# Kernel optimization log

Measured on AMD Instinct MI355X. Metric: run time of the kernel, lower is better.

## Reference

```python
import jax, jax.numpy as jnp
import numpy as np

N = 100000      # nodes
E = 1600000     # edges (before self-loops)
IN = 256        # in_channels
H = 4           # heads (layer 1)
C = 16          # hidden_channels
OUT = 40        # out_channels
NEG_SLOPE = 0.2  # PyG GATConv default


def setup_inputs() -> dict:
    key = jax.random.key(0)
    ks = jax.random.split(key, 10)
    x = jax.random.normal(ks[0], (N, IN), dtype=jnp.float32)
    edge_index = jax.random.randint(ks[1], (2, E), 0, N, dtype=jnp.int64)
    s = 0.1
    return {
        "x": x,
        "edge_index": edge_index,
        "W1": jax.random.normal(ks[2], (IN, H * C), dtype=jnp.float32) * s,
        "a_src1": jax.random.normal(ks[3], (H, C), dtype=jnp.float32) * s,
        "a_dst1": jax.random.normal(ks[4], (H, C), dtype=jnp.float32) * s,
        "b1": jnp.zeros((H * C,), dtype=jnp.float32),
        "W2": jax.random.normal(ks[5], (H * C, OUT), dtype=jnp.float32) * s,
        "a_src2": jax.random.normal(ks[6], (1, OUT), dtype=jnp.float32) * s,
        "a_dst2": jax.random.normal(ks[7], (1, OUT), dtype=jnp.float32) * s,
        "b2": jnp.zeros((OUT,), dtype=jnp.float32),
    }


def gat_conv(x, src, dst, W, a_s, a_d, b, heads, ch, n):
    # x: [n, d_in] -> projected [n, heads, ch]
    xp = (x @ W).reshape(n, heads, ch)
    # per-node attention contributions [n, heads]
    e_s = jnp.einsum('nhc,hc->nh', xp, a_s)
    e_d = jnp.einsum('nhc,hc->nh', xp, a_d)
    # per-edge logits (gather) [E, heads]
    e = jax.nn.leaky_relu(e_s[src] + e_d[dst], negative_slope=NEG_SLOPE)
    # segment softmax over edges sharing a destination node
    m = jax.ops.segment_max(e, dst, num_segments=n)
    m = jnp.where(jnp.isfinite(m), m, 0.0)
    ex = jnp.exp(e - m[dst])
    z = jax.ops.segment_sum(ex, dst, num_segments=n)
    alpha = ex / (z[dst] + 1e-16)               # [E, heads]
    # weighted scatter-add aggregation [n, heads, ch]
    out = jax.ops.segment_sum(xp[src] * alpha[:, :, None], dst, num_segments=n)
    return out.reshape(n, heads * ch) + b       # concat heads + bias


def reference(x, edge_index, W1, a_src1, a_dst1, b1, W2, a_src2, a_dst2, b2):
    n = x.shape[0]
    loop = jnp.arange(n, dtype=edge_index.dtype)
    src = jnp.concatenate([edge_index[0], loop])  # PyG add_self_loops=True
    dst = jnp.concatenate([edge_index[1], loop])
    h = gat_conv(x, src, dst, W1, a_src1, a_dst1, b1, H, C, n)
    h = jax.nn.relu(h)
    out = gat_conv(h, src, dst, W2, a_src2, a_dst2, b2, 1, OUT, n)
    return out
```

## Files before the change

kernel.cpp:

```cpp
#include <hip/hip_runtime.h>
#include <hip/hip_bf16.h>

#define IN_DIM 256
#define HC     64
#define OUT_DIM 40
#define NEG    0.2f

#define NB_SH   8
#define NB_MASK 255
#define SRC_BITS 17
#define SRC_MASK 0x1FFFF
#define CHUNK   8192
#define LEN_CAP 6144

typedef __bf16 bf16x8 __attribute__((ext_vector_type(8)));
typedef float  f32x4  __attribute__((ext_vector_type(4)));

__device__ inline float lrelu(float v) { return fmaxf(v, NEG * v); }

__global__ __launch_bounds__(256) void hist_kernel(
    const int* __restrict__ ei, int* __restrict__ blkhistT, int* __restrict__ btot,
    int E, int ET, int nbuck, int nblk) {
  __shared__ int hist[512];
  int tid = threadIdx.x;
  hist[tid] = 0; hist[tid + 256] = 0;
  __syncthreads();
  int base = blockIdx.x * CHUNK;
  #pragma unroll
  for (int it = 0; it < CHUNK / 1024; ++it) {
    int e = base + it * 1024 + tid * 4;
    if (e + 3 < E) {
      int4 d4 = *(const int4*)&ei[E + e];
      atomicAdd(&hist[d4.x >> NB_SH], 1);
      atomicAdd(&hist[d4.y >> NB_SH], 1);
      atomicAdd(&hist[d4.z >> NB_SH], 1);
      atomicAdd(&hist[d4.w >> NB_SH], 1);
    } else {
      #pragma unroll
      for (int k = 0; k < 4; ++k) {
        int ee = e + k;
        if (ee < ET) {
          int d = (ee < E) ? ei[E + ee] : (ee - E);
          atomicAdd(&hist[d >> NB_SH], 1);
        }
      }
    }
  }
  __syncthreads();
  for (int i = tid; i < nbuck; i += 256) {
    int c = hist[i];
    blkhistT[(size_t)i * nblk + blockIdx.x] = c;
    if (c) atomicAdd(&btot[i], c);
  }
}

__global__ __launch_bounds__(512) void bscan_kernel(
    const int* __restrict__ btot, int* __restrict__ bstart,
    int* __restrict__ offs, int nbuck, int ET, int n) {
  __shared__ int sm[512];
  int tid = threadIdx.x;
  int total = (tid < nbuck) ? btot[tid] : 0;
  sm[tid] = total; __syncthreads();
  for (int o = 1; o < 512; o <<= 1) {
    int v = (tid >= o) ? sm[tid - o] : 0;
    __syncthreads();
    sm[tid] += v;
    __syncthreads();
  }
  if (tid < nbuck) bstart[tid] = sm[tid] - total;
  if (tid == 0) { bstart[nbuck] = ET; offs[n] = ET; }
}

__global__ __launch_bounds__(256) void curs_kernel(
    const int* __restrict__ blkhistT, const int* __restrict__ bstart,
    int* __restrict__ cur, int nblk, int nbuck) {
  __shared__ int sm[256];
  int b = blockIdx.x, tid = threadIdx.x;
  int run = bstart[b];
  for (int c = 0; c < nblk; c += 256) {
    int idx = c + tid;
    int v = (idx < nblk) ? blkhistT[(size_t)b * nblk + idx] : 0;
    sm[tid] = v; __syncthreads();
    for (int o = 1; o < 256; o <<= 1) {
      int x = (tid >= o) ? sm[tid - o] : 0;
      __syncthreads();
      sm[tid] += x;
      __syncthreads();
    }
    if (idx < nblk) cur[(size_t)idx * nbuck + b] = run + sm[tid] - v;
    run += sm[255];
    __syncthreads();
  }
}

__device__ __forceinline__ void gemm1_body(
    char* smem, int tile,
    const float* __restrict__ x, const __bf16* __restrict__ Wt,
    const float* __restrict__ a_s, const float* __restrict__ a_d,
    __bf16* __restrict__ xp1b, float* __restrict__ es1, float* __restrict__ ed1, int n) {
  uint4* wl = (uint4*)smem;
  int tid = threadIdx.x;
  const uint4* gw = (const uint4*)Wt;
  #pragma unroll
  for (int it = 0; it < 4; ++it) {
    int c16 = it * 512 + tid;
    int row = c16 >> 5;
    int swz = c16 ^ (row & 7);
    wl[swz] = gw[c16];
  }
  __syncthreads();

  int wave = tid >> 6, lane = tid & 63;
  int l15 = lane & 15, kgrp = lane >> 4;
  int rowA = tile * 128 + wave * 16 + l15;
  bool okA = rowA < n;
  const float* xrow = x + (size_t)(okA ? rowA : (n - 1)) * IN_DIM;

  f32x4 va[8][2];
  #pragma unroll
  for (int c = 0; c < 8; ++c) {
    int k0 = c * 32 + kgrp * 8;
    va[c][0] = *(const f32x4*)(xrow + k0);
    va[c][1] = *(const f32x4*)(xrow + k0 + 4);
  }
  __builtin_amdgcn_sched_barrier(0);

  f32x4 acc[4] = {};
  #pragma unroll
  for (int c = 0; c < 8; ++c) {
    bf16x8 ahi, alo;
    #pragma unroll
    for (int i = 0; i < 4; ++i) {
      float f0 = va[c][0][i], f1 = va[c][1][i];
      __bf16 h0 = (__bf16)f0, h1 = (__bf16)f1;
      ahi[i]     = h0;
      ahi[4 + i] = h1;
      alo[i]     = (__bf16)(f0 - (float)h0);
      alo[4 + i] = (__bf16)(f1 - (float)h1);
    }
    #pragma unroll
    for (int t = 0; t < 4; ++t) {
      int row  = t * 16 + l15;
      int unit = row * 32 + c * 4 + kgrp;
      int swz  = unit ^ (row & 7);
      bf16x8 b = *(const bf16x8*)&wl[swz];
      acc[t] = __builtin_amdgcn_mfma_f32_16x16x32_bf16(ahi, b, acc[t], 0, 0, 0);
      acc[t] = __builtin_amdgcn_mfma_f32_16x16x32_bf16(alo, b, acc[t], 0, 0, 0);
    }
  }

  int rowbase = tile * 128 + wave * 16 + kgrp * 4;
  #pragma unroll
  for (int t = 0; t < 4; ++t) {
    float as_v = a_s[t * 16 + l15], ad_v = a_d[t * 16 + l15];
    #pragma unroll
    for (int r = 0; r < 4; ++r) {
      int row = rowbase + r;
      float v = acc[t][r];
      bool ok = row < n;
      if (ok) xp1b[(size_t)row * HC + t * 16 + l15] = (__bf16)v;
      float ps = v * as_v, pd = v * ad_v;
      #pragma unroll
      for (int o = 1; o < 16; o <<= 1) {
        ps += __shfl_xor(ps, o, 16);
        pd += __shfl_xor(pd, o, 16);
      }
      if (ok && l15 == 0) {
        es1[row * 4 + t] = ps;
        ed1[row * 4 + t] = pd;
      }
    }
  }
}

__global__ __launch_bounds__(512) void fused_sg(
    const int* __restrict__ ei, const int* __restrict__ cur,
    unsigned int* __restrict__ pairs, int E, int ET, int nbuck, int nsc,
    const float* __restrict__ x, const __bf16* __restrict__ Wt,
    const float* __restrict__ a_s, const float* __restrict__ a_d,
    __bf16* __restrict__ xp1b, float* __restrict__ es1, float* __restrict__ ed1, int n) {
  __shared__ __align__(16) char smem[71680];
  if ((int)blockIdx.x >= nsc) {
    gemm1_body(smem, (int)blockIdx.x - nsc, x, Wt, a_s, a_d, xp1b, es1, ed1, n);
    return;
  }
  int* hs   = (int*)smem;
  int* addb = (int*)(smem + 2048);
  int* lcnt = (int*)(smem + 4096);
  unsigned int* lout = (unsigned int*)(smem + 6144);
  int* ldst = (int*)(smem + 6144 + CHUNK * 4);
  int tid = threadIdx.x, blk = blockIdx.x, base = blk * CHUNK;
  hs[tid] = 0; lcnt[tid] = 0;
  __syncthreads();
  int se[16], de[16];
  #pragma unroll
  for (int it = 0; it < CHUNK / 2048; ++it) {
    int e = base + it * 2048 + tid * 4;
    if (e + 3 < E) {
      int4 s4 = *(const int4*)&ei[e];
      int4 d4 = *(const int4*)&ei[E + e];
      se[it * 4 + 0] = s4.x; de[it * 4 + 0] = d4.x; atomicAdd(&hs[d4.x >> NB_SH], 1);
      se[it * 4 + 1] = s4.y; de[it * 4 + 1] = d4.y; atomicAdd(&hs[d4.y >> NB_SH], 1);
      se[it * 4 + 2] = s4.z; de[it * 4 + 2] = d4.z; atomicAdd(&hs[d4.z >> NB_SH], 1);
      se[it * 4 + 3] = s4.w; de[it * 4 + 3] = d4.w; atomicAdd(&hs[d4.w >> NB_SH], 1);
    } else {
      #pragma unroll
      for (int k = 0; k < 4; ++k) {
        int ee = e + k;
        int s = 0, d = 0;
        if (ee < ET) {
          if (ee < E) { s = ei[ee]; d = ei[E + ee]; }
          else        { s = ee - E; d = s; }
          atomicAdd(&hs[d >> NB_SH], 1);
        }
        se[it * 4 + k] = s; de[it * 4 + k] = d;
      }
    }
  }
  __syncthreads();
  int t = hs[tid];
  for (int o = 1; o < 512; o <<= 1) {
    int v = (tid >= o) ? hs[tid - o] : 0;
    __syncthreads();
    hs[tid] += v;
    __syncthreads();
  }
  int lofs = hs[tid] - t;
  __syncthreads();
  hs[tid] = lofs;
  addb[tid] = ((tid < nbuck) ? cur[(size_t)blk * nbuck + tid] : 0) - lofs;
  __syncthreads();
  #pragma unroll
  for (int it = 0; it < CHUNK / 2048; ++it) {
    #pragma unroll
    for (int k = 0; k < 4; ++k) {
      int e = base + it * 2048 + tid * 4 + k;
      if (e < ET) {
        int b = de[it * 4 + k] >> NB_SH;
        int pos = hs[b] + atomicAdd(&lcnt[b], 1);
        lout[pos] = (unsigned)se[it * 4 + k] |
                    ((unsigned)(de[it * 4 + k] & NB_MASK) << SRC_BITS);
        ldst[pos] = addb[b] + pos;
      }
    }
  }
  __syncthreads();
  int len = min(CHUNK, ET - base);
  for (int i = tid; i < len; i += 512) pairs[ldst[i]] = lout[i];
}

__global__ __launch_bounds__(512) void fused_pg(
    const unsigned int* __restrict__ pairs, const int* __restrict__ bstart,
    int* __restrict__ offs, int* __restrict__ srcs, int n, int nbuck, int tile0,
    const float* __restrict__ x, const __bf16* __restrict__ Wt,
    const float* __restrict__ a_s, const float* __restrict__ a_d,
    __bf16* __restrict__ xp1b, float* __restrict__ es1, float* __restrict__ ed1) {
  __shared__ __align__(16) char smem[53248];
  if ((int)blockIdx.x >= nbuck) {
    gemm1_body(smem, tile0 + (int)blockIdx.x - nbuck, x, Wt, a_s, a_d, xp1b, es1, ed1, n);
    return;
  }
  unsigned int* lin = (unsigned int*)smem;
  unsigned int* lou = (unsigned int*)(smem + 24576);
  int* lhs  = (int*)(smem + 49152);
  int* lcnt = (int*)(smem + 50176);
  int* sm   = (int*)(smem + 51200);
  int b = blockIdx.x, tid = threadIdx.x;
  int rbeg = bstart[b], rend = bstart[b + 1], len = rend - rbeg;
  int node0 = b << NB_SH;
  int nloc = min(256, n - node0);
  if (tid < 256) { lhs[tid] = 0; lcnt[tid] = 0; }
  __syncthreads();
  if (len <= LEN_CAP) {
    for (int i = tid; i < len; i += 512) {
      unsigned p = pairs[rbeg + i];
      lin[i] = p;
      atomicAdd(&lhs[(p >> SRC_BITS) & NB_MASK], 1);
    }
    __syncthreads();
    int t = (tid < 256) ? lhs[tid] : 0;
    sm[tid] = t; __syncthreads();
    for (int o = 1; o < 512; o <<= 1) {
      int v = (tid >= o) ? sm[tid - o] : 0;
      __syncthreads();
      sm[tid] += v;
      __syncthreads();
    }
    int excl = sm[tid] - t;
    if (tid < nloc) offs[node0 + tid] = rbeg + excl;
    if (tid < 256) lhs[tid] = excl;
    __syncthreads();
    for (int i = tid; i < len; i += 512) {
      unsigned p = lin[i];
      int dl = (p >> SRC_BITS) & NB_MASK;
      int pos = lhs[dl] + atomicAdd(&lcnt[dl], 1);
      lou[pos] = p & SRC_MASK;
    }
    __syncthreads();
    for (int i = tid; i < len; i += 512) srcs[rbeg + i] = (int)lou[i];
  } else {
    for (int i = tid; i < len; i += 512)
      atomicAdd(&lhs[(pairs[rbeg + i] >> SRC_BITS) & NB_MASK], 1);
    __syncthreads();
    int t = (tid < 256) ? lhs[tid] : 0;
    sm[tid] = t; __syncthreads();
    for (int o = 1; o < 512; o <<= 1) {
      int v = (tid >= o) ? sm[tid - o] : 0;
      __syncthreads();
      sm[tid] += v;
      __syncthreads();
    }
    int excl = sm[tid] - t;
    if (tid < nloc) offs[node0 + tid] = rbeg + excl;
    if (tid < 256) lhs[tid] = excl;
    __syncthreads();
    for (int i = tid; i < len; i += 512) {
      unsigned p = pairs[rbeg + i];
      int dl = (p >> SRC_BITS) & NB_MASK;
      int pos = lhs[dl] + atomicAdd(&lcnt[dl], 1);
      srcs[rbeg + pos] = (int)(p & SRC_MASK);
    }
  }
}

__global__ void wprep_kernel(const float* __restrict__ W1, __bf16* __restrict__ Wt,
                             int* __restrict__ btot, int nbuck) {
  int i = blockIdx.x * blockDim.x + threadIdx.x;
  if (i < nbuck) btot[i] = 0;
  if (i >= IN_DIM * HC) return;
  int k = i >> 6, nn = i & 63;
  Wt[nn * IN_DIM + k] = (__bf16)W1[i];
}

__global__ __launch_bounds__(256) void agg1_csr(
    const int* __restrict__ offs, const int* __restrict__ srcs,
    const float* __restrict__ es1, const float* __restrict__ ed1,
    const __bf16* __restrict__ xp1b, const float* __restrict__ b1,
    __bf16* __restrict__ hb, int n) {
  __shared__ float lds[4][16 * 4 * 2];
  int wave = threadIdx.x >> 6;
  int wid = (blockIdx.x * 256 + threadIdx.x) >> 6;
  if (wid >= n) return;
  int lane = threadIdx.x & 63;
  int eidx = lane >> 2, hA = lane & 3;
  int a = lane & 31, half = lane >> 5;
  int ch0 = a * 2, headB = a >> 3;
  int beg = offs[wid], end = offs[wid + 1];
  float edh = ed1[wid * 4 + hA];
  float zacc = 0.f, acc0 = 0.f, acc1 = 0.f;
  const char* xbase = (const char*)xp1b + ch0 * 2;
  float* myl = lds[wave];

  for (int e0 = beg; e0 < end; e0 += 16) {
    int cnt = min(16, end - e0);
    float ex = 0.f;
    int s = 0;
    if (eidx < cnt) {
      s = srcs[e0 + eidx];
      ex = __expf(lrelu(es1[s * 4 + hA] + edh));
    }
    zacc += ex;
    myl[lane * 2]     = ex;
    myl[lane * 2 + 1] = __int_as_float(s * (int)(HC * sizeof(__bf16)));
    if (cnt == 16) {
      float2 ao[8];
      #pragma unroll
      for (int jp = 0; jp < 8; ++jp)
        ao[jp] = *(const float2*)&myl[((jp * 2 + half) * 4 + headB) * 2];
      unsigned wj[8];
      #pragma unroll
      for (int jp = 0; jp < 8; ++jp)
        wj[jp] = *(const unsigned*)(xbase + __float_as_int(ao[jp].y));
      #pragma unroll
      for (int jp = 0; jp < 8; ++jp) {
        float f0 = __int_as_float((int)(wj[jp] << 16));
        float f1 = __int_as_float((int)(wj[jp] & 0xffff0000u));
        acc0 = fmaf(ao[jp].x, f0, acc0);
        acc1 = fmaf(ao[jp].x, f1, acc1);
      }
    } else {
      int jpmax = (cnt + 1 - half) >> 1;
      #pragma unroll 4
      for (int jp = 0; jp < jpmax; ++jp) {
        float2 ao = *(const float2*)&myl[((jp * 2 + half) * 4 + headB) * 2];
        unsigned w = *(const unsigned*)(xbase + __float_as_int(ao.y));
        float f0 = __int_as_float((int)(w << 16));
        float f1 = __int_as_float((int)(w & 0xffff0000u));
        acc0 = fmaf(ao.x, f0, acc0);
        acc1 = fmaf(ao.x, f1, acc1);
      }
    }
  }

  float z = zacc;
  z += __shfl_xor(z, 4); z += __shfl_xor(z, 8);
  z += __shfl_xor(z, 16); z += __shfl_xor(z, 32);
  float zc = __shfl(z, headB);
  acc0 += __shfl_xor(acc0, 32);
  acc1 += __shfl_xor(acc1, 32);
  if (half == 0) {
    float inv = 1.f / (zc + 1e-16f);
    __bf16 r0 = (__bf16)fmaxf(fmaf(acc0, inv, b1[ch0]), 0.f);
    __bf16 r1 = (__bf16)fmaxf(fmaf(acc1, inv, b1[ch0 + 1]), 0.f);
    unsigned pk = ((unsigned)*(unsigned short*)&r0) |
                  (((unsigned)*(unsigned short*)&r1) << 16);
    *(unsigned*)&hb[(size_t)wid * HC + ch0] = pk;
  }
}

__global__ __launch_bounds__(256) void layer2_mfma(
    const __bf16* __restrict__ hb, const float* __restrict__ W2,
    const float* __restrict__ a_s2, const float* __restrict__ a_d2,
    __bf16* __restrict__ xp2b, float* __restrict__ es2, float* __restrict__ ed2, int n) {
  int tid = threadIdx.x;
  int wave = tid >> 6, lane = tid & 63;
  int l15 = lane & 15, kgrp = lane >> 4;
  int rowA = blockIdx.x * 64 + wave * 16 + l15;
  const __bf16* hrow = hb + (size_t)(rowA < n ? rowA : (n - 1)) * HC;

  bf16x8 av[2];
  av[0] = *(const bf16x8*)(hrow + kgrp * 8);
  av[1] = *(const bf16x8*)(hrow + 32 + kgrp * 8);

  f32x4 acc[3] = {};
  #pragma unroll
  for (int c = 0; c < 2; ++c) {
    #pragma unroll
    for (int t = 0; t < 3; ++t) {
      int col = t * 16 + l15;
      bool okc = col < OUT_DIM;
      bf16x8 bhi, blo;
      #pragma unroll
      for (int i = 0; i < 8; ++i) {
        int k = c * 32 + kgrp * 8 + i;
        float w = okc ? W2[k * OUT_DIM + col] : 0.f;
        __bf16 wh = (__bf16)w;
        bhi[i] = wh;
        blo[i] = (__bf16)(w - (float)wh);
      }
      acc[t] = __builtin_amdgcn_mfma_f32_16x16x32_bf16(av[c], bhi, acc[t], 0, 0, 0);
      acc[t] = __builtin_amdgcn_mfma_f32_16x16x32_bf16(av[c], blo, acc[t], 0, 0, 0);
    }
  }

  int rowbase = blockIdx.x * 64 + wave * 16 + kgrp * 4;
  #pragma unroll
  for (int r = 0; r < 4; ++r) {
    int row = rowbase + r;
    bool ok = row < n;
    float ps = 0.f, pd = 0.f;
    #pragma unroll
    for (int t = 0; t < 3; ++t) {
      int col = t * 16 + l15;
      if (col < OUT_DIM) {
        float v = acc[t][r];
        if (ok) xp2b[(size_t)row * OUT_DIM + col] = (__bf16)v;
        ps = fmaf(v, a_s2[col], ps);
        pd = fmaf(v, a_d2[col], pd);
      }
    }
    #pragma unroll
    for (int o = 1; o < 16; o <<= 1) {
      ps += __shfl_xor(ps, o, 16);
      pd += __shfl_xor(pd, o, 16);
    }
    if (ok && l15 == 0) { es2[row] = ps; ed2[row] = pd; }
  }
}

__global__ __launch_bounds__(256) void agg2_csr(
    const int* __restrict__ offs, const int* __restrict__ srcs,
    const float* __restrict__ es2, const float* __restrict__ ed2,
    const __bf16* __restrict__ xp2b, const float* __restrict__ b2,
    float* __restrict__ out, int n) {
  __shared__ float lds[4][64 * 2];
  int wave = threadIdx.x >> 6;
  int wid = (blockIdx.x * 256 + threadIdx.x) >> 6;
  if (wid >= n) return;
  int lane = threadIdx.x & 63;
  int a = lane & 31, half = lane >> 5;
  int ch0 = a * 2;
  int beg = offs[wid], end = offs[wid + 1];
  float edv = ed2[wid];
  float zacc = 0.f, acc0 = 0.f, acc1 = 0.f;
  const char* xbase = (const char*)xp2b + ch0 * 2;
  float* myl = lds[wave];

  for (int e0 = beg; e0 < end; e0 += 64) {
    int cnt = min(64, end - e0);
    float ex = 0.f;
    int s = 0;
    if (lane < cnt) {
      s = srcs[e0 + lane];
      ex = __expf(lrelu(es2[s] + edv));
    }
    zacc += ex;
    myl[lane * 2]     = ex;
    myl[lane * 2 + 1] = __int_as_float(s * (int)(OUT_DIM * sizeof(__bf16)));
    if (a < 20) {
      int jpmax = (cnt + 1 - half) >> 1;
      int jp = 0;
      for (; jp + 8 <= jpmax; jp += 8) {
        float2 ao[8];
        #pragma unroll
        for (int k = 0; k < 8; ++k)
          ao[k] = *(const float2*)&myl[((jp + k) * 2 + half) * 2];
        unsigned wj[8];
        #pragma unroll
        for (int k = 0; k < 8; ++k)
          wj[k] = *(const unsigned*)(xbase + __float_as_int(ao[k].y));
        #pragma unroll
        for (int k = 0; k < 8; ++k) {
          float f0 = __int_as_float((int)(wj[k] << 16));
          float f1 = __int_as_float((int)(wj[k] & 0xffff0000u));
          acc0 = fmaf(ao[k].x, f0, acc0);
          acc1 = fmaf(ao[k].x, f1, acc1);
        }
      }
      #pragma unroll 4
      for (; jp < jpmax; ++jp) {
        float2 ao = *(const float2*)&myl[(jp * 2 + half) * 2];
        unsigned w = *(const unsigned*)(xbase + __float_as_int(ao.y));
        float f0 = __int_as_float((int)(w << 16));
        float f1 = __int_as_float((int)(w & 0xffff0000u));
        acc0 = fmaf(ao.x, f0, acc0);
        acc1 = fmaf(ao.x, f1, acc1);
      }
    }
  }

  float z = zacc;
  #pragma unroll
  for (int o = 1; o < 64; o <<= 1) z += __shfl_xor(z, o);
  acc0 += __shfl_xor(acc0, 32);
  acc1 += __shfl_xor(acc1, 32);
  if (half == 0 && a < 20) {
    float inv = 1.f / (z + 1e-16f);
    float2 r;
    r.x = fmaf(acc0, inv, b2[ch0]);
    r.y = fmaf(acc1, inv, b2[ch0 + 1]);
    *(float2*)&out[(size_t)wid * OUT_DIM + ch0] = r;
  }
}

extern "C" void kernel_launch(void* const* d_in, const int* in_sizes, int n_in,
                              void* d_out, int out_size, void* d_ws, size_t ws_size,
                              hipStream_t stream) {
  const float* x    = (const float*)d_in[0];
  const int*   ei   = (const int*)d_in[1];
  const float* W1   = (const float*)d_in[2];
  const float* a_s1 = (const float*)d_in[3];
  const float* a_d1 = (const float*)d_in[4];
  const float* b1   = (const float*)d_in[5];
  const float* W2   = (const float*)d_in[6];
  const float* a_s2 = (const float*)d_in[7];
  const float* a_d2 = (const float*)d_in[8];
  const float* b2   = (const float*)d_in[9];

  int n  = in_sizes[0] / IN_DIM;
  int E  = in_sizes[1] / 2;
  int ET = E + n;
  int nbuck = (n + 255) >> NB_SH;
  int nblk1 = (ET + CHUNK - 1) / CHUNK;
  int ntile = (n + 127) / 128;
  int t0 = ntile / 2;
  float* out = (float*)d_out;

  char* ws = (char*)d_ws;
  size_t off = 0;
  auto alloc = [&](size_t bytes) -> void* {
    void* p = ws + off;
    off = (off + bytes + 255) & ~(size_t)255;
    return p;
  };
  __bf16* xp1b     = (__bf16*)alloc((size_t)n * HC * 2);
  __bf16* xp2b     = (__bf16*)alloc((size_t)n * OUT_DIM * 2);
  __bf16* hb       = (__bf16*)alloc((size_t)n * HC * 2);
  float*  es1      = (float*)alloc((size_t)n * 4 * 4);
  float*  ed1      = (float*)alloc((size_t)n * 4 * 4);
  float*  es2      = (float*)alloc((size_t)n * 4);
  float*  ed2      = (float*)alloc((size_t)n * 4);
  int*    blkhistT = (int*)alloc((size_t)nblk1 * nbuck * 4);
  int*    cur      = (int*)alloc((size_t)nblk1 * nbuck * 4);
  int*    btot     = (int*)alloc((size_t)(nbuck + 1) * 4);
  int*    bstart   = (int*)alloc((size_t)(nbuck + 1) * 4);
  int*    offs     = (int*)alloc((size_t)(n + 1) * 4);
  int*    srcs     = (int*)alloc((size_t)ET * 4);
  unsigned int* pairs = (unsigned int*)alloc((size_t)ET * 4);
  __bf16* Wt       = (__bf16*)alloc((size_t)IN_DIM * HC * 2);

  wprep_kernel<<<(IN_DIM * HC + 255) / 256, 256, 0, stream>>>(W1, Wt, btot, nbuck);
  hist_kernel<<<nblk1, 256, 0, stream>>>(ei, blkhistT, btot, E, ET, nbuck, nblk1);
  bscan_kernel<<<1, 512, 0, stream>>>(btot, bstart, offs, nbuck, ET, n);
  curs_kernel<<<nbuck, 256, 0, stream>>>(blkhistT, bstart, cur, nblk1, nbuck);
  fused_sg<<<nblk1 + t0, 512, 0, stream>>>(ei, cur, pairs, E, ET, nbuck, nblk1,
                                           x, Wt, a_s1, a_d1, xp1b, es1, ed1, n);
  fused_pg<<<nbuck + (ntile - t0), 512, 0, stream>>>(pairs, bstart, offs, srcs, n, nbuck, t0,
                                                     x, Wt, a_s1, a_d1, xp1b, es1, ed1);
  agg1_csr<<<(n * 64 + 255) / 256, 256, 0, stream>>>(offs, srcs, es1, ed1, xp1b, b1, hb, n);
  layer2_mfma<<<(n + 63) / 64, 256, 0, stream>>>(hb, W2, a_s2, a_d2, xp2b, es2, ed2, n);
  agg2_csr<<<(n * 64 + 255) / 256, 256, 0, stream>>>(offs, srcs, es2, ed2, xp2b, b2, out, n);
}
```

Baseline: 185.7 us.

## Spread layer-1 GEMM tiles across histogram, cursor, scatter and pair kernels

The layer-1 projection GEMM tiles were previously co-scheduled only with the scatter and pair-grouping kernels. They are now split across four CSR-build launches (histogram, cursor scan, scatter, pair), with tile fractions set by fixed ratios. The histogram and cursor kernels move to 512-thread blocks so they can share a block shape with the GEMM body. The aim is to fill idle CUs during the small, latency-bound histogram and scan kernels, at the cost of possibly lengthening those kernels if the GEMM blocks delay the critical path.

Result: slower. 194.8 us (+4.9%).

```diff
diff --git a/kernel.cpp b/kernel.cpp
--- a/kernel.cpp
+++ b/kernel.cpp
@@ -18,17 +18,105 @@
 
 __device__ inline float lrelu(float v) { return fmaxf(v, NEG * v); }
 
-__global__ __launch_bounds__(256) void hist_kernel(
+__device__ __forceinline__ void gemm1_body(
+    char* smem, int tile,
+    const float* __restrict__ x, const __bf16* __restrict__ Wt,
+    const float* __restrict__ a_s, const float* __restrict__ a_d,
+    __bf16* __restrict__ xp1b, float* __restrict__ es1, float* __restrict__ ed1, int n) {
+  uint4* wl = (uint4*)smem;
+  int tid = threadIdx.x;
+  const uint4* gw = (const uint4*)Wt;
+  #pragma unroll
+  for (int it = 0; it < 4; ++it) {
+    int c16 = it * 512 + tid;
+    int row = c16 >> 5;
+    int swz = c16 ^ (row & 7);
+    wl[swz] = gw[c16];
+  }
+  __syncthreads();
+
+  int wave = tid >> 6, lane = tid & 63;
+  int l15 = lane & 15, kgrp = lane >> 4;
+  int rowA = tile * 128 + wave * 16 + l15;
+  bool okA = rowA < n;
+  const float* xrow = x + (size_t)(okA ? rowA : (n - 1)) * IN_DIM;
+
+  f32x4 va[8][2];
+  #pragma unroll
+  for (int c = 0; c < 8; ++c) {
+    int k0 = c * 32 + kgrp * 8;
+    va[c][0] = *(const f32x4*)(xrow + k0);
+    va[c][1] = *(const f32x4*)(xrow + k0 + 4);
+  }
+  __builtin_amdgcn_sched_barrier(0);
+
+  f32x4 acc[4] = {};
+  #pragma unroll
+  for (int c = 0; c < 8; ++c) {
+    bf16x8 ahi, alo;
+    #pragma unroll
+    for (int i = 0; i < 4; ++i) {
+      float f0 = va[c][0][i], f1 = va[c][1][i];
+      __bf16 h0 = (__bf16)f0, h1 = (__bf16)f1;
+      ahi[i]     = h0;
+      ahi[4 + i] = h1;
+      alo[i]     = (__bf16)(f0 - (float)h0);
+      alo[4 + i] = (__bf16)(f1 - (float)h1);
+    }
+    #pragma unroll
+    for (int t = 0; t < 4; ++t) {
+      int row  = t * 16 + l15;
+      int unit = row * 32 + c * 4 + kgrp;
+      int swz  = unit ^ (row & 7);
+      bf16x8 b = *(const bf16x8*)&wl[swz];
+      acc[t] = __builtin_amdgcn_mfma_f32_16x16x32_bf16(ahi, b, acc[t], 0, 0, 0);
+      acc[t] = __builtin_amdgcn_mfma_f32_16x16x32_bf16(alo, b, acc[t], 0, 0, 0);
+    }
+  }
+
+  int rowbase = tile * 128 + wave * 16 + kgrp * 4;
+  #pragma unroll
+  for (int t = 0; t < 4; ++t) {
+    float as_v = a_s[t * 16 + l15], ad_v = a_d[t * 16 + l15];
+    #pragma unroll
+    for (int r = 0; r < 4; ++r) {
+      int row = rowbase + r;
+      float v = acc[t][r];
+      bool ok = row < n;
+      if (ok) xp1b[(size_t)row * HC + t * 16 + l15] = (__bf16)v;
+      float ps = v * as_v, pd = v * ad_v;
+      #pragma unroll
+      for (int o = 1; o < 16; o <<= 1) {
+        ps += __shfl_xor(ps, o, 16);
+        pd += __shfl_xor(pd, o, 16);
+      }
+      if (ok && l15 == 0) {
+        es1[row * 4 + t] = ps;
+        ed1[row * 4 + t] = pd;
+      }
+    }
+  }
+}
+
+__global__ __launch_bounds__(512) void fused_hg(
     const int* __restrict__ ei, int* __restrict__ blkhistT, int* __restrict__ btot,
-    int E, int ET, int nbuck, int nblk) {
-  __shared__ int hist[512];
-  int tid = threadIdx.x;
-  hist[tid] = 0; hist[tid + 256] = 0;
-  __syncthreads();
-  int base = blockIdx.x * CHUNK;
-  #pragma unroll
-  for (int it = 0; it < CHUNK / 1024; ++it) {
-    int e = base + it * 1024 + tid * 4;
+    int E, int ET, int nbuck, int nblk,
+    const float* __restrict__ x, const __bf16* __restrict__ Wt,
+    const float* __restrict__ a_s, const float* __restrict__ a_d,
+    __bf16* __restrict__ xp1b, float* __restrict__ es1, float* __restrict__ ed1, int n) {
+  __shared__ __align__(16) char smem[32768];
+  if ((int)blockIdx.x >= nblk) {
+    gemm1_body(smem, (int)blockIdx.x - nblk, x, Wt, a_s, a_d, xp1b, es1, ed1, n);
+    return;
+  }
+  int* hist = (int*)smem;
+  int tid = threadIdx.x, blk = blockIdx.x;
+  hist[tid] = 0;
+  __syncthreads();
+  int base = blk * CHUNK;
+  #pragma unroll
+  for (int it = 0; it < CHUNK / 2048; ++it) {
+    int e = base + it * 2048 + tid * 4;
     if (e + 3 < E) {
       int4 d4 = *(const int4*)&ei[E + e];
       atomicAdd(&hist[d4.x >> NB_SH], 1);
@@ -47,9 +135,9 @@
     }
   }
   __syncthreads();
-  for (int i = tid; i < nbuck; i += 256) {
+  for (int i = tid; i < nbuck; i += 512) {
     int c = hist[i];
-    blkhistT[(size_t)i * nblk + blockIdx.x] = c;
+    blkhistT[(size_t)i * nblk + blk] = c;
     if (c) atomicAdd(&btot[i], c);
   }
 }
@@ -71,117 +159,45 @@
   if (tid == 0) { bstart[nbuck] = ET; offs[n] = ET; }
 }
 
-__global__ __launch_bounds__(256) void curs_kernel(
+__global__ __launch_bounds__(512) void fused_cg(
     const int* __restrict__ blkhistT, const int* __restrict__ bstart,
-    int* __restrict__ cur, int nblk, int nbuck) {
-  __shared__ int sm[256];
+    int* __restrict__ cur, int nblk, int nbuck, int tile0,
+    const float* __restrict__ x, const __bf16* __restrict__ Wt,
+    const float* __restrict__ a_s, const float* __restrict__ a_d,
+    __bf16* __restrict__ xp1b, float* __restrict__ es1, float* __restrict__ ed1, int n) {
+  __shared__ __align__(16) char smem[32768];
+  if ((int)blockIdx.x >= nbuck) {
+    gemm1_body(smem, tile0 + (int)blockIdx.x - nbuck, x, Wt, a_s, a_d, xp1b, es1, ed1, n);
+    return;
+  }
+  int* sm = (int*)smem;
   int b = blockIdx.x, tid = threadIdx.x;
   int run = bstart[b];
-  for (int c = 0; c < nblk; c += 256) {
+  for (int c = 0; c < nblk; c += 512) {
     int idx = c + tid;
     int v = (idx < nblk) ? blkhistT[(size_t)b * nblk + idx] : 0;
     sm[tid] = v; __syncthreads();
-    for (int o = 1; o < 256; o <<= 1) {
-      int x = (tid >= o) ? sm[tid - o] : 0;
+    for (int o = 1; o < 512; o <<= 1) {
+      int x2 = (tid >= o) ? sm[tid - o] : 0;
       __syncthreads();
-      sm[tid] += x;
+      sm[tid] += x2;
       __syncthreads();
     }
     if (idx < nblk) cur[(size_t)idx * nbuck + b] = run + sm[tid] - v;
-    run += sm[255];
-    __syncthreads();
-  }
-}
-
-__device__ __forceinline__ void gemm1_body(
-    char* smem, int tile,
-    const float* __restrict__ x, const __bf16* __restrict__ Wt,
-    const float* __restrict__ a_s, const float* __restrict__ a_d,
-    __bf16* __restrict__ xp1b, float* __restrict__ es1, float* __restrict__ ed1, int n) {
-  uint4* wl = (uint4*)smem;
-  int tid = threadIdx.x;
-  const uint4* gw = (const uint4*)Wt;
-  #pragma unroll
-  for (int it = 0; it < 4; ++it) {
-    int c16 = it * 512 + tid;
-    int row = c16 >> 5;
-    int swz = c16 ^ (row & 7);
-    wl[swz] = gw[c16];
-  }
-  __syncthreads();
-
-  int wave = tid >> 6, lane = tid & 63;
-  int l15 = lane & 15, kgrp = lane >> 4;
-  int rowA = tile * 128 + wave * 16 + l15;
-  bool okA = rowA < n;
-  const float* xrow = x + (size_t)(okA ? rowA : (n - 1)) * IN_DIM;
-
-  f32x4 va[8][2];
-  #pragma unroll
-  for (int c = 0; c < 8; ++c) {
-    int k0 = c * 32 + kgrp * 8;
-    va[c][0] = *(const f32x4*)(xrow + k0);
-    va[c][1] = *(const f32x4*)(xrow + k0 + 4);
-  }
-  __builtin_amdgcn_sched_barrier(0);
-
-  f32x4 acc[4] = {};
-  #pragma unroll
-  for (int c = 0; c < 8; ++c) {
-    bf16x8 ahi, alo;
-    #pragma unroll
-    for (int i = 0; i < 4; ++i) {
-      float f0 = va[c][0][i], f1 = va[c][1][i];
-      __bf16 h0 = (__bf16)f0, h1 = (__bf16)f1;
-      ahi[i]     = h0;
-      ahi[4 + i] = h1;
-      alo[i]     = (__bf16)(f0 - (float)h0);
-      alo[4 + i] = (__bf16)(f1 - (float)h1);
-    }
-    #pragma unroll
-    for (int t = 0; t < 4; ++t) {
-      int row  = t * 16 + l15;
-      int unit = row * 32 + c * 4 + kgrp;
-      int swz  = unit ^ (row & 7);
-      bf16x8 b = *(const bf16x8*)&wl[swz];
-      acc[t] = __builtin_amdgcn_mfma_f32_16x16x32_bf16(ahi, b, acc[t], 0, 0, 0);
-      acc[t] = __builtin_amdgcn_mfma_f32_16x16x32_bf16(alo, b, acc[t], 0, 0, 0);
-    }
-  }
-
-  int rowbase = tile * 128 + wave * 16 + kgrp * 4;
-  #pragma unroll
-  for (int t = 0; t < 4; ++t) {
-    float as_v = a_s[t * 16 + l15], ad_v = a_d[t * 16 + l15];
-    #pragma unroll
-    for (int r = 0; r < 4; ++r) {
-      int row = rowbase + r;
-      float v = acc[t][r];
-      bool ok = row < n;
-      if (ok) xp1b[(size_t)row * HC + t * 16 + l15] = (__bf16)v;
-      float ps = v * as_v, pd = v * ad_v;
-      #pragma unroll
-      for (int o = 1; o < 16; o <<= 1) {
-        ps += __shfl_xor(ps, o, 16);
-        pd += __shfl_xor(pd, o, 16);
-      }
-      if (ok && l15 == 0) {
-        es1[row * 4 + t] = ps;
-        ed1[row * 4 + t] = pd;
-      }
-    }
+    run += sm[511];
+    __syncthreads();
   }
 }
 
 __global__ __launch_bounds__(512) void fused_sg(
     const int* __restrict__ ei, const int* __restrict__ cur,
-    unsigned int* __restrict__ pairs, int E, int ET, int nbuck, int nsc,
+    unsigned int* __restrict__ pairs, int E, int ET, int nbuck, int nsc, int tile0,
     const float* __restrict__ x, const __bf16* __restrict__ Wt,
     const float* __restrict__ a_s, const float* __restrict__ a_d,
     __bf16* __restrict__ xp1b, float* __restrict__ es1, float* __restrict__ ed1, int n) {
   __shared__ __align__(16) char smem[71680];
   if ((int)blockIdx.x >= nsc) {
-    gemm1_body(smem, (int)blockIdx.x - nsc, x, Wt, a_s, a_d, xp1b, es1, ed1, n);
+    gemm1_body(smem, tile0 + (int)blockIdx.x - nsc, x, Wt, a_s, a_d, xp1b, es1, ed1, n);
     return;
   }
   int* hs   = (int*)smem;
@@ -563,7 +579,10 @@
   int nbuck = (n + 255) >> NB_SH;
   int nblk1 = (ET + CHUNK - 1) / CHUNK;
   int ntile = (n + 127) / 128;
-  int t0 = ntile / 2;
+  int ta = (ntile * 29) / 100;
+  int tb = (ntile * 29) / 100;
+  int tc = (ntile * 21) / 100;
+  int td = ntile - ta - tb - tc;
   float* out = (float*)d_out;
 
   char* ws = (char*)d_ws;
@@ -590,13 +609,15 @@
   __bf16* Wt       = (__bf16*)alloc((size_t)IN_DIM * HC * 2);
 
   wprep_kernel<<<(IN_DIM * HC + 255) / 256, 256, 0, stream>>>(W1, Wt, btot, nbuck);
-  hist_kernel<<<nblk1, 256, 0, stream>>>(ei, blkhistT, btot, E, ET, nbuck, nblk1);
+  fused_hg<<<nblk1 + ta, 512, 0, stream>>>(ei, blkhistT, btot, E, ET, nbuck, nblk1,
+                                           x, Wt, a_s1, a_d1, xp1b, es1, ed1, n);
   bscan_kernel<<<1, 512, 0, stream>>>(btot, bstart, offs, nbuck, ET, n);
-  curs_kernel<<<nbuck, 256, 0, stream>>>(blkhistT, bstart, cur, nblk1, nbuck);
-  fused_sg<<<nblk1 + t0, 512, 0, stream>>>(ei, cur, pairs, E, ET, nbuck, nblk1,
+  fused_cg<<<nbuck + tb, 512, 0, stream>>>(blkhistT, bstart, cur, nblk1, nbuck, ta,
                                            x, Wt, a_s1, a_d1, xp1b, es1, ed1, n);
-  fused_pg<<<nbuck + (ntile - t0), 512, 0, stream>>>(pairs, bstart, offs, srcs, n, nbuck, t0,
-                                                     x, Wt, a_s1, a_d1, xp1b, es1, ed1);
+  fused_sg<<<nblk1 + tc, 512, 0, stream>>>(ei, cur, pairs, E, ET, nbuck, nblk1, ta + tb,
+                                           x, Wt, a_s1, a_d1, xp1b, es1, ed1, n);
+  fused_pg<<<nbuck + td, 512, 0, stream>>>(pairs, bstart, offs, srcs, n, nbuck, ta + tb + tc,
+                                           x, Wt, a_s1, a_d1, xp1b, es1, ed1);
   agg1_csr<<<(n * 64 + 255) / 256, 256, 0, stream>>>(offs, srcs, es1, ed1, xp1b, b1, hb, n);
   layer2_mfma<<<(n + 63) / 64, 256, 0, stream>>>(hb, W2, a_s2, a_d2, xp2b, es2, ed2, n);
   agg2_csr<<<(n * 64 + 255) / 256, 256, 0, stream>>>(offs, srcs, es2, ed2, xp2b, b2, out, n);
```
